# Performance work log

Hardware: AMD Instinct MI355X
Metric: run time of the kernel (lower is better)

The kernel has to match this reference:

```python
import jax, jax.numpy as jnp
import numpy as np

B, S, D, H = 2, 2048, 1024, 16
DK = D // H


def setup_inputs() -> dict:
    key = jax.random.key(0)
    ks = jax.random.split(key, 12)
    scale = 0.02
    inp = {
        "query": jax.random.normal(ks[0], (B, S, D), jnp.float32),
        "key": jax.random.normal(ks[1], (B, S, D), jnp.float32),
        "value": jax.random.normal(ks[2], (B, S, D), jnp.float32),
        "mask": jax.random.randint(ks[3], (B, S), 0, 2, jnp.int32),
        "Wq": jax.random.normal(ks[4], (D, D), jnp.float32) * scale,
        "bq": jnp.zeros((D,), jnp.float32),
        "Wk": jax.random.normal(ks[5], (D, D), jnp.float32) * scale,
        "bk": jnp.zeros((D,), jnp.float32),
        "Wv": jax.random.normal(ks[6], (D, D), jnp.float32) * scale,
        "bv": jnp.zeros((D,), jnp.float32),
        "Wo": jax.random.normal(ks[7], (D, D), jnp.float32) * scale,
        "bo": jnp.zeros((D,), jnp.float32),
    }
    return inp


def reference(query, key, value, mask, Wq, bq, Wk, bk, Wv, bv, Wo, bo):
    # Linear projections then split heads: [B, S, D] -> [B, H, S, DK]
    def proj(x, W, b):
        y = x @ W.T + b  # torch nn.Linear: x @ W^T + b
        return y.reshape(B, S, H, DK).transpose(0, 2, 1, 3)

    q = proj(query, Wq, bq)
    k = proj(key, Wk, bk)
    v = proj(value, Wv, bv)

    # Scaled dot-product attention with full [B, H, S, S] scores (naive form)
    scores = jnp.einsum("bhqd,bhkd->bhqk", q, k) / jnp.sqrt(jnp.float32(DK))
    # mask==1 marks padding over key positions; broadcast [B,1,1,S]
    pad = (mask == 1)[:, None, None, :]
    scores = jnp.where(pad, -jnp.inf, scores)
    p_attn = jax.nn.softmax(scores, axis=-1)
    # dropout omitted (eval / deterministic mode)
    x = jnp.einsum("bhqk,bhkd->bhqd", p_attn, v)
    x = x.transpose(0, 2, 1, 3).reshape(B, S, D)
    return x @ Wo.T + bo
```

## Files before the change

kernel.cpp:

```cpp
#include <hip/hip_runtime.h>
#include <stdint.h>
#include <type_traits>

typedef short bf16x8 __attribute__((ext_vector_type(8)));
typedef float f32x4  __attribute__((ext_vector_type(4)));
typedef unsigned int u32x2 __attribute__((ext_vector_type(2)));
typedef unsigned short u16;

#define BB 2
#define SS 2048
#define DD 1024
#define HH 16
#define NTOK (BB*SS)
#define QSC 0.18033688f

__device__ __forceinline__ u16 f2bf(float f) {
  union { float f; uint32_t u; } c; c.f = f;
  uint32_t r = c.u + 0x7FFFu + ((c.u >> 16) & 1u);
  return (u16)(r >> 16);
}

__device__ __forceinline__ void gll16(const void* g, void* l) {
  __builtin_amdgcn_global_load_lds((__attribute__((address_space(1))) void*)(void*)g,
                                   (__attribute__((address_space(3))) void*)l, 16, 0, 0);
}

struct PrepArgs {
  const float* src[7]; u16* dst[7]; int n[7];
  const int* mask; float* padcnt;
};
__global__ __launch_bounds__(256) void prep_kernel(PrepArgs a) {
  const int y = blockIdx.y;
  if (y < 7) {
    const float* __restrict__ src = a.src[y];
    u16* __restrict__ dst = a.dst[y];
    const int n = a.n[y];
    int i = (blockIdx.x * blockDim.x + threadIdx.x) * 4;
    const int stride = gridDim.x * blockDim.x * 4;
    for (; i < n; i += stride) {
      float4 v = *(const float4*)(src + i);
      ushort4 o;
      o.x = f2bf(v.x); o.y = f2bf(v.y); o.z = f2bf(v.z); o.w = f2bf(v.w);
      *(ushort4*)(dst + i) = o;
    }
  } else {
    if (blockIdx.x >= BB) return;
    const int b = blockIdx.x, t = threadIdx.x;
    const int4 v1 = *(const int4*)(a.mask + b * SS + t * 8);
    const int4 v2 = *(const int4*)(a.mask + b * SS + t * 8 + 4);
    int s = v1.x + v1.y + v1.z + v1.w + v2.x + v2.y + v2.z + v2.w;
#pragma unroll
    for (int off = 32; off; off >>= 1) s += __shfl_xor(s, off);
    __shared__ int red[4];
    if ((t & 63) == 0) red[t >> 6] = s;
    __syncthreads();
    if (t == 0) a.padcnt[b] = (float)(red[0] + red[1] + red[2] + red[3]);
  }
}

template<int MODE>
__device__ __forceinline__ void gemm_bt_body(const u16* __restrict__ A,
                                             const u16* __restrict__ W,
                                             const float* __restrict__ bias,
                                             const int* __restrict__ mask,
                                             void* __restrict__ Cout,
                                             int m0, int n0,
                                             u16* As, u16* Bs) {
  const int tid = threadIdx.x;
  const int lane = tid & 63, wid = tid >> 6;
  const int r16 = lane & 15, g4 = lane >> 4;
  const int wm = (wid >> 1) * 64, wn = (wid & 1) * 64;

  const f32x4 zero = {0.f, 0.f, 0.f, 0.f};
  f32x4 acc[4][4];
#pragma unroll
  for (int i = 0; i < 4; ++i)
#pragma unroll
    for (int j = 0; j < 4; ++j) acc[i][j] = zero;

  const int row0 = tid >> 2, blk0 = tid & 3;
  auto stage = [&](int kt, int buf) {
#pragma unroll
    for (int it = 0; it < 2; ++it) {
      const int row = row0 + it * 64;
      const int sb = blk0 ^ (row & 3);
      gll16(A + (size_t)(m0 + row) * DD + kt * 32 + sb * 8,
            As + buf * 4096 + (tid + it * 256) * 8);
      gll16(W + (size_t)(n0 + row) * DD + kt * 32 + sb * 8,
            Bs + buf * 4096 + (tid + it * 256) * 8);
    }
  };

  stage(0, 0);
  __syncthreads();

  for (int kt = 0; kt < DD / 32; ++kt) {
    const int cur = kt & 1;
    if (kt + 1 < DD / 32) stage(kt + 1, cur ^ 1);

    bf16x8 af[4], bfr[4];
#pragma unroll
    for (int i = 0; i < 4; ++i) {
      const int ar = wm + i * 16 + r16;
      af[i] = *(const bf16x8*)(As + cur * 4096 + ar * 32 + ((g4 ^ (ar & 3)) << 3));
      const int br = wn + i * 16 + r16;
      bfr[i] = *(const bf16x8*)(Bs + cur * 4096 + br * 32 + ((g4 ^ (br & 3)) << 3));
    }
#pragma unroll
    for (int i = 0; i < 4; ++i)
#pragma unroll
      for (int j = 0; j < 4; ++j)
        acc[i][j] = __builtin_amdgcn_mfma_f32_16x16x32_bf16(af[i], bfr[j], acc[i][j], 0, 0, 0);
    __syncthreads();
  }

  float bcol[4];
#pragma unroll
  for (int j = 0; j < 4; ++j) bcol[j] = bias[n0 + wn + j * 16 + r16];

#pragma unroll
  for (int i = 0; i < 4; ++i) {
    const int rowb = m0 + wm + i * 16 + g4 * 4;
    int mr[4] = {0, 0, 0, 0};
    if (MODE == 1 || MODE == 2) {
      const int4 mv = *(const int4*)(mask + rowb);
      mr[0] = mv.x; mr[1] = mv.y; mr[2] = mv.z; mr[3] = mv.w;
    }
#pragma unroll
    for (int j = 0; j < 4; ++j) {
      const int col = n0 + wn + j * 16 + r16;
      if (MODE == 3) {
#pragma unroll
        for (int r = 0; r < 4; ++r)
          ((float*)Cout)[(size_t)(rowb + r) * DD + col] = acc[i][j][r] + bcol[j];
      } else if (MODE == 0) {
#pragma unroll
        for (int r = 0; r < 4; ++r)
          ((u16*)Cout)[(size_t)(rowb + r) * DD + col] = f2bf((acc[i][j][r] + bcol[j]) * QSC);
      } else if (MODE == 1) {
#pragma unroll
        for (int r = 0; r < 4; ++r) {
          const float v = mr[r] ? 0.f : (acc[i][j][r] + bcol[j]);
          ((u16*)Cout)[(size_t)(rowb + r) * DD + col] = f2bf(v);
        }
      } else {
        const int bb = rowb >> 11, s0 = rowb & (SS - 1);
        ushort4 pk;
        pk.x = f2bf(mr[0] ? 0.f : (acc[i][j][0] + bcol[j]));
        pk.y = f2bf(mr[1] ? 0.f : (acc[i][j][1] + bcol[j]));
        pk.z = f2bf(mr[2] ? 0.f : (acc[i][j][2] + bcol[j]));
        pk.w = f2bf(mr[3] ? 0.f : (acc[i][j][3] + bcol[j]));
        *(ushort4*)((u16*)Cout + (size_t)(bb * DD + col) * SS + s0) = pk;
      }
    }
  }
}

struct QkvArgs {
  const u16* A[3];
  const u16* W[3];
  const float* bias[3];
  const int* mask;
  u16* outq; u16* outk; u16* outv;
};

__global__ __launch_bounds__(256) void gemm_qkv_kernel(QkvArgs a) {
  __shared__ __align__(16) u16 As[2][4096];
  __shared__ __align__(16) u16 Bs[2][4096];
  const int fid = blockIdx.x + (blockIdx.y << 3) + (blockIdx.z << 8);
  const int swz = (fid & 7) * 96 + (fid >> 3);
  const int z = swz >> 8;
  const int rem = swz & 255;
  const int m0 = (rem >> 3) * 128, n0 = (rem & 7) * 128;
  if (z == 0)      gemm_bt_body<0>(a.A[0], a.W[0], a.bias[0], nullptr, (void*)a.outq, m0, n0, &As[0][0], &Bs[0][0]);
  else if (z == 1) gemm_bt_body<1>(a.A[1], a.W[1], a.bias[1], a.mask, (void*)a.outk, m0, n0, &As[0][0], &Bs[0][0]);
  else             gemm_bt_body<2>(a.A[2], a.W[2], a.bias[2], a.mask, (void*)a.outv, m0, n0, &As[0][0], &Bs[0][0]);
}

__global__ __launch_bounds__(256) void gemm_out_kernel(const u16* __restrict__ A,
                                                       const u16* __restrict__ W,
                                                       const float* __restrict__ bias,
                                                       float* __restrict__ C) {
  __shared__ __align__(16) u16 As[2][4096];
  __shared__ __align__(16) u16 Bs[2][4096];
  const int fid = blockIdx.x + (blockIdx.y << 3);
  const int swz = (fid & 7) * 32 + (fid >> 3);
  const int m0 = (swz >> 3) * 128, n0 = (swz & 7) * 128;
  gemm_bt_body<3>(A, W, bias, nullptr, (void*)C, m0, n0, &As[0][0], &Bs[0][0]);
}

#define NT (SS / 64)
__global__ __launch_bounds__(256) void attn_kernel(const u16* __restrict__ Qp,
                                                   const u16* __restrict__ Kp,
                                                   const u16* __restrict__ Vt,
                                                   const float* __restrict__ padcnt,
                                                   u16* __restrict__ ctx) {
  __shared__ __align__(16) u16 Ks[2][64 * 64];
  __shared__ __align__(16) u16 Vs[2][64 * 64];

  const int tid = threadIdx.x;
  const int lane = tid & 63, wid = tid >> 6;
  const int r16 = lane & 15, g4 = lane >> 4;
  const int fid = blockIdx.x + 32 * (blockIdx.y + 16 * blockIdx.z);
  const int swz = (fid & 7) * 128 + (fid >> 3);
  const int qt = swz & 31, rem = swz >> 5;
  const int h = rem & 15, b = rem >> 4;

  const int qtok = b * SS + qt * 64 + wid * 16 + r16;
  bf16x8 qf[2];
#pragma unroll
  for (int c = 0; c < 2; ++c)
    qf[c] = *(const bf16x8*)(Qp + (size_t)qtok * DD + h * 64 + c * 32 + g4 * 8);

  const f32x4 zero = {0.f, 0.f, 0.f, 0.f};
  f32x4 o[4];
#pragma unroll
  for (int j = 0; j < 4; ++j) o[j] = zero;
  float ll = 0.f;

  const u16* kptr[2];
  const u16* vptr[2];
  {
    const int srow0 = tid >> 3, sblk0 = tid & 7;
#pragma unroll
    for (int it = 0; it < 2; ++it) {
      const int row = srow0 + it * 32;
      const int sb = sblk0 ^ (row & 7);
      kptr[it] = Kp + (size_t)(b * SS + row) * DD + h * 64 + sb * 8;
      vptr[it] = Vt + (size_t)(b * DD + h * 64 + row) * SS + sb * 8;
    }
  }
  auto stage = [&](int buf) {
#pragma unroll
    for (int it = 0; it < 2; ++it) {
      gll16(kptr[it], &Ks[buf][(tid + it * 256) * 8]);
      gll16(vptr[it], &Vs[buf][(tid + it * 256) * 8]);
      kptr[it] += 64 * DD;
      vptr[it] += 64;
    }
  };

  stage(0);
  __syncthreads();

  auto tile_step = [&](auto CURC, int kt) {
    constexpr int cur = decltype(CURC)::value;
    if (kt + 1 < NT) stage(cur ^ 1);

    f32x4 st[4];
    __builtin_amdgcn_s_setprio(1);
#pragma unroll
    for (int j = 0; j < 4; ++j) {
      const int kr = j * 16 + r16;
      const bf16x8 kf = *(const bf16x8*)(&Ks[cur][kr * 64 + ((g4 ^ (kr & 7)) << 3)]);
      st[j] = __builtin_amdgcn_mfma_f32_16x16x32_bf16(kf, qf[0], zero, 0, 0, 0);
    }
#pragma unroll
    for (int j = 0; j < 4; ++j) {
      const int kr = j * 16 + r16;
      const bf16x8 kf = *(const bf16x8*)(&Ks[cur][kr * 64 + (((4 + g4) ^ (kr & 7)) << 3)]);
      st[j] = __builtin_amdgcn_mfma_f32_16x16x32_bf16(kf, qf[1], st[j], 0, 0, 0);
    }
    __builtin_amdgcn_s_setprio(0);

    uint32_t q0[4], q1[4];
#pragma unroll
    for (int j = 0; j < 4; ++j) {
      float p0, p1, p2, p3;
      asm("v_exp_f32 %0, %1" : "=v"(p0) : "v"(st[j][0]));
      asm("v_exp_f32 %0, %1" : "=v"(p1) : "v"(st[j][1]));
      asm("v_exp_f32 %0, %1" : "=v"(p2) : "v"(st[j][2]));
      asm("v_exp_f32 %0, %1" : "=v"(p3) : "v"(st[j][3]));
      ll += (p0 + p1) + (p2 + p3);
      asm("v_cvt_pk_bf16_f32 %0, %1, %2" : "=v"(q0[j]) : "v"(p0), "v"(p1));
      asm("v_cvt_pk_bf16_f32 %0, %1, %2" : "=v"(q1[j]) : "v"(p2), "v"(p3));
    }

    bf16x8 pa[2];
#pragma unroll
    for (int c = 0; c < 2; ++c) {
      u32x2 s0 = __builtin_amdgcn_permlane32_swap(q0[2 * c], q0[2 * c + 1], false, false);
      u32x2 s1 = __builtin_amdgcn_permlane16_swap(s0.x, s0.y, false, false);
      u32x2 t0 = __builtin_amdgcn_permlane32_swap(q1[2 * c], q1[2 * c + 1], false, false);
      u32x2 t1 = __builtin_amdgcn_permlane16_swap(t0.x, t0.y, false, false);
      union { uint32_t u[4]; bf16x8 v; } cv;
      cv.u[0] = s1.x; cv.u[1] = t1.x; cv.u[2] = s1.y; cv.u[3] = t1.y;
      pa[c] = cv.v;
    }

    __builtin_amdgcn_s_setprio(1);
#pragma unroll
    for (int c = 0; c < 2; ++c)
#pragma unroll
      for (int j = 0; j < 4; ++j) {
        const int vr = j * 16 + r16;
        const bf16x8 vf = *(const bf16x8*)(&Vs[cur][vr * 64 + (((c * 4 + g4) ^ (vr & 7)) << 3)]);
        o[j] = __builtin_amdgcn_mfma_f32_16x16x32_bf16(pa[c], vf, o[j], 0, 0, 0);
      }
    __builtin_amdgcn_s_setprio(0);
    __syncthreads();
  };

  for (int kt = 0; kt < NT; kt += 2) {
    tile_step(std::integral_constant<int, 0>{}, kt);
    tile_step(std::integral_constant<int, 1>{}, kt + 1);
  }

  ll += __shfl_xor(ll, 16);
  ll += __shfl_xor(ll, 32);
  ll -= padcnt[b];
  const float inv = 1.0f / ll;
  float invr[4];
#pragma unroll
  for (int r = 0; r < 4; ++r) invr[r] = __shfl(inv, g4 * 4 + r);

  const int otok = b * SS + qt * 64 + wid * 16 + g4 * 4;
#pragma unroll
  for (int j = 0; j < 4; ++j) {
    const int col = h * 64 + j * 16 + r16;
#pragma unroll
    for (int r = 0; r < 4; ++r)
      ctx[(size_t)(otok + r) * DD + col] = f2bf(o[j][r] * invr[r]);
  }
}

extern "C" void kernel_launch(void* const* d_in, const int* in_sizes, int n_in,
                              void* d_out, int out_size, void* d_ws, size_t ws_size,
                              hipStream_t stream) {
  (void)in_sizes; (void)n_in; (void)out_size; (void)ws_size;
  const float* f_q = (const float*)d_in[0];
  const float* f_k = (const float*)d_in[1];
  const float* f_v = (const float*)d_in[2];
  const int* mask  = (const int*)d_in[3];
  const float* Wq = (const float*)d_in[4];
  const float* bq = (const float*)d_in[5];
  const float* Wk = (const float*)d_in[6];
  const float* bk = (const float*)d_in[7];
  const float* Wv = (const float*)d_in[8];
  const float* bv = (const float*)d_in[9];
  const float* Wo = (const float*)d_in[10];
  const float* bo = (const float*)d_in[11];

  char* ws = (char*)d_ws;
  const size_t XB = (size_t)NTOK * DD * 2;
  const size_t WB = (size_t)DD * DD * 2;
  u16* Xq  = (u16*)(ws);
  u16* Xk  = (u16*)(ws + XB);
  u16* Xv  = (u16*)(ws + 2 * XB);
  u16* Qp  = (u16*)(ws + 3 * XB);
  u16* Kp  = (u16*)(ws + 4 * XB);
  u16* Vt  = (u16*)(ws + 5 * XB);
  u16* Wqb = (u16*)(ws + 6 * XB);
  u16* Wkb = (u16*)(ws + 6 * XB + WB);
  u16* Wvb = (u16*)(ws + 6 * XB + 2 * WB);
  u16* Wob = (u16*)(ws + 6 * XB + 3 * WB);
  float* padcnt = (float*)(ws + 6 * XB + 4 * WB);
  u16* ctx = Xq;

  PrepArgs pa;
  pa.src[0] = f_q; pa.src[1] = f_k; pa.src[2] = f_v;
  pa.src[3] = Wq;  pa.src[4] = Wk;  pa.src[5] = Wv;  pa.src[6] = Wo;
  pa.dst[0] = Xq;  pa.dst[1] = Xk;  pa.dst[2] = Xv;
  pa.dst[3] = Wqb; pa.dst[4] = Wkb; pa.dst[5] = Wvb; pa.dst[6] = Wob;
  pa.n[0] = pa.n[1] = pa.n[2] = NTOK * DD;
  pa.n[3] = pa.n[4] = pa.n[5] = pa.n[6] = DD * DD;
  pa.mask = mask; pa.padcnt = padcnt;
  prep_kernel<<<dim3(1024, 8), 256, 0, stream>>>(pa);

  QkvArgs qa;
  qa.A[0] = Xq;  qa.A[1] = Xk;  qa.A[2] = Xv;
  qa.W[0] = Wqb; qa.W[1] = Wkb; qa.W[2] = Wvb;
  qa.bias[0] = bq; qa.bias[1] = bk; qa.bias[2] = bv;
  qa.mask = mask;
  qa.outq = Qp; qa.outk = Kp; qa.outv = Vt;
  gemm_qkv_kernel<<<dim3(DD / 128, NTOK / 128, 3), 256, 0, stream>>>(qa);

  attn_kernel<<<dim3(SS / 64, HH, BB), 256, 0, stream>>>(Qp, Kp, Vt, padcnt, ctx);
  gemm_out_kernel<<<dim3(DD / 128, NTOK / 128), 256, 0, stream>>>(ctx, Wob, bo, (float*)d_out);
}
```

Baseline: 138.9 us.

## Keep two loads in flight with explicit vmcnt waits in GEMM and attention loops

```diff
diff --git a/kernel.cpp b/kernel.cpp
--- a/kernel.cpp
+++ b/kernel.cpp
@@ -6,6 +6,9 @@
 typedef float f32x4  __attribute__((ext_vector_type(4)));
 typedef unsigned int u32x2 __attribute__((ext_vector_type(2)));
 typedef unsigned short u16;
+
+template<int N> using ic = std::integral_constant<int, N>;
+template<bool B> using bc = std::integral_constant<bool, B>;
 
 #define BB 2
 #define SS 2048
@@ -78,26 +81,37 @@
 #pragma unroll
     for (int j = 0; j < 4; ++j) acc[i][j] = zero;
 
-  const int row0 = tid >> 2, blk0 = tid & 3;
-  auto stage = [&](int kt, int buf) {
+  const u16* aptr[2];
+  const u16* wptr[2];
+  {
+    const int row0 = tid >> 2, blk0 = tid & 3;
 #pragma unroll
     for (int it = 0; it < 2; ++it) {
       const int row = row0 + it * 64;
       const int sb = blk0 ^ (row & 3);
-      gll16(A + (size_t)(m0 + row) * DD + kt * 32 + sb * 8,
-            As + buf * 4096 + (tid + it * 256) * 8);
-      gll16(W + (size_t)(n0 + row) * DD + kt * 32 + sb * 8,
-            Bs + buf * 4096 + (tid + it * 256) * 8);
+      aptr[it] = A + (size_t)(m0 + row) * DD + sb * 8;
+      wptr[it] = W + (size_t)(n0 + row) * DD + sb * 8;
+    }
+  }
+  auto stage = [&](int buf) {
+#pragma unroll
+    for (int it = 0; it < 2; ++it) {
+      gll16(aptr[it], As + buf * 4096 + (tid + it * 256) * 8);
+      gll16(wptr[it], Bs + buf * 4096 + (tid + it * 256) * 8);
+      aptr[it] += 32; wptr[it] += 32;
     }
   };
 
-  stage(0, 0);
-  __syncthreads();
-
-  for (int kt = 0; kt < DD / 32; ++kt) {
-    const int cur = kt & 1;
-    if (kt + 1 < DD / 32) stage(kt + 1, cur ^ 1);
-
+  stage(0);
+  stage(1);
+
+  auto kstep = [&](auto CURC, auto VMC, auto STGC) {
+    constexpr int cur = decltype(CURC)::value;
+    constexpr int vm  = decltype(VMC)::value;
+    constexpr bool stg = decltype(STGC)::value;
+    asm volatile("s_waitcnt vmcnt(%0)" :: "n"(vm) : "memory");
+    __builtin_amdgcn_s_barrier();
+    __builtin_amdgcn_sched_barrier(0);
     bf16x8 af[4], bfr[4];
 #pragma unroll
     for (int i = 0; i < 4; ++i) {
@@ -111,8 +125,17 @@
 #pragma unroll
       for (int j = 0; j < 4; ++j)
         acc[i][j] = __builtin_amdgcn_mfma_f32_16x16x32_bf16(af[i], bfr[j], acc[i][j], 0, 0, 0);
-    __syncthreads();
-  }
+    __builtin_amdgcn_sched_barrier(0);
+    __builtin_amdgcn_s_barrier();
+    if constexpr (stg) stage(cur);
+  };
+
+  for (int kt = 0; kt < DD / 32 - 2; kt += 2) {
+    kstep(ic<0>{}, ic<4>{}, bc<true>{});
+    kstep(ic<1>{}, ic<4>{}, bc<true>{});
+  }
+  kstep(ic<0>{}, ic<4>{}, bc<false>{});
+  kstep(ic<1>{}, ic<0>{}, bc<false>{});
 
   float bcol[4];
 #pragma unroll
@@ -241,11 +264,15 @@
   };
 
   stage(0);
-  __syncthreads();
-
-  auto tile_step = [&](auto CURC, int kt) {
+  stage(1);
+
+  auto tile_step = [&](auto CURC, auto VMC, auto STGC) {
     constexpr int cur = decltype(CURC)::value;
-    if (kt + 1 < NT) stage(cur ^ 1);
+    constexpr int vm  = decltype(VMC)::value;
+    constexpr bool stg = decltype(STGC)::value;
+    asm volatile("s_waitcnt vmcnt(%0)" :: "n"(vm) : "memory");
+    __builtin_amdgcn_s_barrier();
+    __builtin_amdgcn_sched_barrier(0);
 
     f32x4 st[4];
     __builtin_amdgcn_s_setprio(1);
@@ -298,13 +325,17 @@
         o[j] = __builtin_amdgcn_mfma_f32_16x16x32_bf16(pa[c], vf, o[j], 0, 0, 0);
       }
     __builtin_amdgcn_s_setprio(0);
-    __syncthreads();
+    __builtin_amdgcn_sched_barrier(0);
+    __builtin_amdgcn_s_barrier();
+    if constexpr (stg) stage(cur);
   };
 
-  for (int kt = 0; kt < NT; kt += 2) {
-    tile_step(std::integral_constant<int, 0>{}, kt);
-    tile_step(std::integral_constant<int, 1>{}, kt + 1);
-  }
+  for (int kt = 0; kt < NT - 2; kt += 2) {
+    tile_step(ic<0>{}, ic<4>{}, bc<true>{});
+    tile_step(ic<1>{}, ic<4>{}, bc<true>{});
+  }
+  tile_step(ic<0>{}, ic<4>{}, bc<false>{});
+  tile_step(ic<1>{}, ic<0>{}, bc<false>{});
 
   ll += __shfl_xor(ll, 16);
   ll += __shfl_xor(ll, 32);
```

Measured after the change: 140.2 us. About the same (+0.9%).
